# Kernel optimization log

Measured on AMD Instinct MI355X. Metric: run time of the kernel, lower is better.

The kernel has to match this reference:

```python
import jax, jax.numpy as jnp
import numpy as np

DIM = 384
NUM_HEADS = 6
HEAD_DIM = DIM // NUM_HEADS
SCALE = HEAD_DIM ** -0.5


def setup_inputs() -> dict:
    key = jax.random.key(0)
    k_x, k_qkvw, k_qkvb, k_pw, k_pb = jax.random.split(key, 5)
    B, N, C = 8, 2048, DIM
    x = jax.random.normal(k_x, (B, N, C), dtype=jnp.float32)
    # nn.Linear weights stored as (out, in); apply as x @ W.T + b
    s = 1.0 / np.sqrt(C)
    qkv_w = jax.random.uniform(k_qkvw, (3 * C, C), minval=-s, maxval=s, dtype=jnp.float32)
    qkv_b = jax.random.uniform(k_qkvb, (3 * C,), minval=-s, maxval=s, dtype=jnp.float32)
    proj_w = jax.random.uniform(k_pw, (C, C), minval=-s, maxval=s, dtype=jnp.float32)
    proj_b = jax.random.uniform(k_pb, (C,), minval=-s, maxval=s, dtype=jnp.float32)
    return {"x": x, "qkv_w": qkv_w, "qkv_b": qkv_b, "proj_w": proj_w,
            "proj_b": proj_b, "h": 64, "w": 32}


def reference(x, qkv_w, qkv_b, proj_w, proj_b, h, w):
    B, N, C = x.shape
    H, D = NUM_HEADS, HEAD_DIM
    qkv = x @ qkv_w.T + qkv_b              # [B, N, 3C]
    qkv = qkv.reshape(B, N, 3, H, D)
    q = qkv[:, :, 0].transpose(0, 2, 1, 3) * SCALE  # [B, H, N, D]
    k = qkv[:, :, 1].transpose(0, 2, 1, 3)
    v = qkv[:, :, 2].transpose(0, 2, 1, 3)
    attn = jnp.einsum('bhnd,bhmd->bhnm', q, k)      # [B, H, N, N]
    attn = jax.nn.softmax(attn, axis=-1)
    out = jnp.einsum('bhnm,bhmd->bhnd', attn, v)    # [B, H, N, D]
    out = out.transpose(0, 2, 1, 3).reshape(B, N, C)
    return out @ proj_w.T + proj_b
```

## Files before the change

### kernel.cpp

```cpp
#include <hip/hip_runtime.h>

typedef __attribute__((ext_vector_type(8))) short bf16x8;
typedef __attribute__((ext_vector_type(4))) float f32x4;
typedef __attribute__((ext_vector_type(16))) float f32x16;
typedef __attribute__((ext_vector_type(4))) unsigned int u32x4;

#define DIMC 384
#define NHEADS 6
#define HDIM 64
#define BATCH 8
#define SEQ 2048
#define TOKENS (BATCH*SEQ)
#define QKV_OUT (3*DIMC)

__device__ __forceinline__ unsigned short f2bf(float f) {
  unsigned int u = __float_as_uint(f);
  u += 0x7fffu + ((u >> 16) & 1u);
  return (unsigned short)(u >> 16);
}

__device__ __forceinline__ unsigned int cvt_pk_bf16(float a, float b) {
  unsigned int r;
  asm volatile("v_cvt_pk_bf16_f32 %0, %1, %2" : "=v"(r) : "v"(a), "v"(b));
  return r;
}

__device__ __forceinline__ void async_load16(const void* g, void* l) {
  __builtin_amdgcn_global_load_lds(
      (const __attribute__((address_space(1))) unsigned int*)g,
      (__attribute__((address_space(3))) unsigned int*)l, 16, 0, 0);
}

#define N4_X   (TOKENS*DIMC/4)
#define N4_W1  (QKV_OUT*DIMC/4)
#define N4_W2  (DIMC*DIMC/4)
__global__ void cast3_kernel(const float* __restrict__ x,
                             const float* __restrict__ w1,
                             const float* __restrict__ w2,
                             unsigned short* __restrict__ ox,
                             unsigned short* __restrict__ o1,
                             unsigned short* __restrict__ o2) {
  int i = blockIdx.x * blockDim.x + threadIdx.x;
  const int stride = gridDim.x * blockDim.x;
  for (; i < N4_X + N4_W1 + N4_W2; i += stride) {
    const float* src; unsigned short* dst; int j = i;
    if (j < N4_X)            { src = x;  dst = ox; }
    else if (j < N4_X+N4_W1) { j -= N4_X; src = w1; dst = o1; }
    else                     { j -= N4_X+N4_W1; src = w2; dst = o2; }
    float4 v = ((const float4*)src)[j];
    ushort4 o;
    o.x = f2bf(v.x); o.y = f2bf(v.y); o.z = f2bf(v.z); o.w = f2bf(v.w);
    ((ushort4*)dst)[j] = o;
  }
}

__global__ __launch_bounds__(256) void qkv_gemm_kernel(
    const unsigned short* __restrict__ A,
    const unsigned short* __restrict__ W,
    const float* __restrict__ bias,
    unsigned short* __restrict__ Qb,
    unsigned short* __restrict__ Kb,
    unsigned short* __restrict__ Vtb) {
  __shared__ unsigned short As[2][128*32];
  __shared__ unsigned short Bs[2][128*32];
  const int tid = threadIdx.x;
  const int w = tid >> 6, l = tid & 63;
  const int wm = w >> 1, wn = w & 1;
  const int q4 = l >> 4, r15 = l & 15;
  const int m0 = blockIdx.y * 128;
  const int n0 = blockIdx.x * 128;

  f32x4 acc[4][4];
#pragma unroll
  for (int i = 0; i < 4; i++)
#pragma unroll
    for (int j = 0; j < 4; j++) acc[i][j] = f32x4{0.f, 0.f, 0.f, 0.f};

  const int arow = l >> 2;
  const int achk = l & 3;
  const unsigned short* Asrc = A + (size_t)(m0 + w*16 + arow) * 384 + achk * 8;
  const unsigned short* Wsrc = W + (size_t)(n0 + w*16 + arow) * 384 + achk * 8;

#pragma unroll
  for (int cc = 0; cc < 2; ++cc) {
    async_load16(Asrc + cc*64*384, (char*)As[0] + cc*4096 + w*1024);
    async_load16(Wsrc + cc*64*384, (char*)Bs[0] + cc*4096 + w*1024);
  }

  for (int kt = 0; kt < 12; ++kt) {
    const int buf = kt & 1;
    if (kt < 11) {
#pragma unroll
      for (int cc = 0; cc < 2; ++cc) {
        async_load16(Asrc + (kt+1)*32 + cc*64*384, (char*)As[buf^1] + cc*4096 + w*1024);
        async_load16(Wsrc + (kt+1)*32 + cc*64*384, (char*)Bs[buf^1] + cc*4096 + w*1024);
      }
      asm volatile("s_waitcnt vmcnt(4)" ::: "memory");
    } else {
      asm volatile("s_waitcnt vmcnt(0)" ::: "memory");
    }
    __builtin_amdgcn_s_barrier();
    asm volatile("" ::: "memory");
    bf16x8 a[4], b[4];
#pragma unroll
    for (int mi = 0; mi < 4; mi++)
      a[mi] = *(const bf16x8*)(&As[buf][(wm*64 + mi*16 + r15)*32 + q4*8]);
#pragma unroll
    for (int ni = 0; ni < 4; ni++)
      b[ni] = *(const bf16x8*)(&Bs[buf][(wn*64 + ni*16 + r15)*32 + q4*8]);
    __builtin_amdgcn_s_setprio(1);
#pragma unroll
    for (int mi = 0; mi < 4; mi++)
#pragma unroll
      for (int ni = 0; ni < 4; ni++)
        acc[mi][ni] = __builtin_amdgcn_mfma_f32_16x16x32_bf16(
            a[mi], b[ni], acc[mi][ni], 0, 0, 0);
    __builtin_amdgcn_s_setprio(0);
    asm volatile("s_waitcnt lgkmcnt(0)" ::: "memory");
    __builtin_amdgcn_s_barrier();
    asm volatile("" ::: "memory");
  }
  const int c3 = blockIdx.x / 3;
  const int nrel0 = (blockIdx.x % 3) * 128 + wn * 64;
  if (c3 == 2) {
#pragma unroll
    for (int ni = 0; ni < 4; ni++) {
      int ncol = nrel0 + ni*16 + r15;
      float bv = bias[n0 + wn*64 + ni*16 + r15];
      int h = ncol >> 6, d = ncol & 63;
#pragma unroll
      for (int mi = 0; mi < 4; mi++) {
        int m = m0 + wm*64 + mi*16 + 4*q4;
        int bb = m >> 11, t = m & 2047;
        ushort4 pk;
        pk.x = f2bf(acc[mi][ni][0] + bv);
        pk.y = f2bf(acc[mi][ni][1] + bv);
        pk.z = f2bf(acc[mi][ni][2] + bv);
        pk.w = f2bf(acc[mi][ni][3] + bv);
        *(ushort4*)(Vtb + ((size_t)(bb*NHEADS + h)*HDIM + d)*SEQ + t) = pk;
      }
    }
  } else {
    unsigned short* D = (c3 == 0) ? Qb : Kb;
    const float scale = (c3 == 0) ? 0.125f * 1.4426950408889634f : 1.0f;
#pragma unroll
    for (int ni = 0; ni < 4; ni++) {
      int ncol = nrel0 + ni*16 + r15;
      float bv = bias[n0 + wn*64 + ni*16 + r15];
      int h = ncol >> 6, d = ncol & 63;
#pragma unroll
      for (int mi = 0; mi < 4; mi++) {
#pragma unroll
        for (int reg = 0; reg < 4; reg++) {
          int m = m0 + wm*64 + mi*16 + 4*q4 + reg;
          int bb = m >> 11, t = m & 2047;
          float v = (acc[mi][ni][reg] + bv) * scale;
          D[((size_t)(bb*NHEADS + h)*SEQ + t)*HDIM + d] = f2bf(v);
        }
      }
    }
  }
}

__global__ __launch_bounds__(256, 3) void flash_kernel(
    const unsigned short* __restrict__ Q, const unsigned short* __restrict__ K,
    const unsigned short* __restrict__ Vt, unsigned short* __restrict__ O2) {
  __shared__ unsigned short Ks[2][64*64];
  __shared__ unsigned short Vs[2][64*64];
  const int tid = threadIdx.x;
  const int w = tid >> 6, l = tid & 63;
  const int hl = l >> 5, l31 = l & 31, l7 = l & 7;
  const int wg = blockIdx.x;
  const int logical = (wg & 7) * 96 + (wg >> 3);
  const int qt = logical & 15, bh = logical >> 4;
  const unsigned short* Qp = Q  + (size_t)bh * SEQ * HDIM;
  const unsigned short* Kp = K  + (size_t)bh * SEQ * HDIM;
  const unsigned short* Vp = Vt + (size_t)bh * HDIM * SEQ;

  const int qrow = qt*128 + w*32 + l31;
  bf16x8 qf[4];
#pragma unroll
  for (int ks = 0; ks < 4; ks++)
    qf[ks] = *(const bf16x8*)(Qp + (size_t)qrow*HDIM + ks*16 + hl*8);

  const int srow = w*8 + (l >> 3);
  const int sch  = l7 ^ (l >> 3) ^ w;
  const unsigned short* Ksrc = Kp + (size_t)srow*HDIM + sch*8;
  const unsigned short* Vsrc = Vp + (size_t)srow*SEQ  + sch*8;
  char* kdst = (char*)&Ks[0][0] + w*1024;
  char* vdst = (char*)&Vs[0][0] + w*1024;

  const int swl = (l31 >> 3) & 3;
  int rdoff[4];
#pragma unroll
  for (int ks = 0; ks < 4; ks++)
    rdoff[ks] = l31*128 + (((ks*2 + hl) ^ l7 ^ swl) << 4);

  f32x16 o0 = {}, o1 = {};
  float l_run = 0.f;

  async_load16(Ksrc,           kdst);
  async_load16(Ksrc + 32*HDIM, kdst + 4096);
  async_load16(Vsrc,           vdst);
  async_load16(Vsrc + 32*SEQ,  vdst + 4096);

#pragma unroll 2
  for (int kt = 0; kt < 32; ++kt) {
    const int buf = kt & 1;
    const unsigned short* ksb = &Ks[buf][0];
    const unsigned short* vsb = &Vs[buf][0];
    if (kt < 31) {
      const unsigned short* ks_ = Ksrc + (size_t)(kt+1)*64*HDIM;
      const unsigned short* vs_ = Vsrc + (size_t)(kt+1)*64;
      char* kd = kdst + (buf^1)*8192;
      char* vd = vdst + (buf^1)*8192;
      async_load16(ks_,           kd);
      async_load16(ks_ + 32*HDIM, kd + 4096);
      async_load16(vs_,           vd);
      async_load16(vs_ + 32*SEQ,  vd + 4096);
      asm volatile("s_waitcnt vmcnt(4)" ::: "memory");
    } else {
      asm volatile("s_waitcnt vmcnt(0)" ::: "memory");
    }
    __builtin_amdgcn_s_barrier();
    asm volatile("" ::: "memory");

    f32x16 s0 = {}, s1 = {};
    __builtin_amdgcn_s_setprio(1);
#pragma unroll
    for (int ks = 0; ks < 4; ks++) {
      bf16x8 kf0 = *(const bf16x8*)((const char*)ksb + rdoff[ks]);
      bf16x8 kf1 = *(const bf16x8*)((const char*)ksb + 4096 + rdoff[ks]);
      s0 = __builtin_amdgcn_mfma_f32_32x32x16_bf16(kf0, qf[ks], s0, 0, 0, 0);
      s1 = __builtin_amdgcn_mfma_f32_32x32x16_bf16(kf1, qf[ks], s1, 0, 0, 0);
    }
    __builtin_amdgcn_s_setprio(0);

    unsigned int Y[2][4][2];
    float lsum = 0.f;
#pragma unroll
    for (int h = 0; h < 4; h++) {
      float a0 = __builtin_amdgcn_exp2f(s0[4*h+0]);
      float a1 = __builtin_amdgcn_exp2f(s0[4*h+1]);
      float a2 = __builtin_amdgcn_exp2f(s0[4*h+2]);
      float a3 = __builtin_amdgcn_exp2f(s0[4*h+3]);
      lsum += (a0+a1)+(a2+a3);
      Y[0][h][0] = cvt_pk_bf16(a0, a1);
      Y[0][h][1] = cvt_pk_bf16(a2, a3);
      float b0 = __builtin_amdgcn_exp2f(s1[4*h+0]);
      float b1 = __builtin_amdgcn_exp2f(s1[4*h+1]);
      float b2 = __builtin_amdgcn_exp2f(s1[4*h+2]);
      float b3 = __builtin_amdgcn_exp2f(s1[4*h+3]);
      lsum += (b0+b1)+(b2+b3);
      Y[1][h][0] = cvt_pk_bf16(b0, b1);
      Y[1][h][1] = cvt_pk_bf16(b2, b3);
    }
    l_run += lsum;

    bf16x8 pa[4];
#pragma unroll
    for (int ksl = 0; ksl < 4; ksl++) {
      const int kb = ksl >> 1, P2 = ksl & 1;
      unsigned int x0 = Y[kb][2*P2+0][0], x1 = Y[kb][2*P2+0][1];
      unsigned int y0 = Y[kb][2*P2+1][0], y1 = Y[kb][2*P2+1][1];
      asm volatile("v_permlane32_swap_b32 %0, %1" : "+v"(x0), "+v"(y0));
      asm volatile("v_permlane32_swap_b32 %0, %1" : "+v"(x1), "+v"(y1));
      u32x4 t; t[0] = x0; t[1] = x1; t[2] = y0; t[3] = y1;
      union { u32x4 u; bf16x8 b; } cvt; cvt.u = t;
      pa[ksl] = cvt.b;
    }

    __builtin_amdgcn_s_setprio(1);
#pragma unroll
    for (int ksl = 0; ksl < 4; ksl++) {
      bf16x8 vf0 = *(const bf16x8*)((const char*)vsb + rdoff[ksl]);
      bf16x8 vf1 = *(const bf16x8*)((const char*)vsb + 4096 + rdoff[ksl]);
      o0 = __builtin_amdgcn_mfma_f32_32x32x16_bf16(pa[ksl], vf0, o0, 0, 0, 0);
      o1 = __builtin_amdgcn_mfma_f32_32x32x16_bf16(pa[ksl], vf1, o1, 0, 0, 0);
    }
    __builtin_amdgcn_s_setprio(0);
    asm volatile("s_waitcnt lgkmcnt(0)" ::: "memory");
    __builtin_amdgcn_s_barrier();
    asm volatile("" ::: "memory");
  }

  l_run += __shfl_xor(l_run, 32, 64);
  const float linv = 1.0f / l_run;
  const int b = bh / NHEADS, h = bh % NHEADS;
#pragma unroll
  for (int reg = 0; reg < 16; reg++) {
    const int qr = (reg & 3) + 8*(reg >> 2) + 4*hl;
    const float lr = __shfl(linv, qr, 64);
    const int t = qt*128 + w*32 + qr;
    unsigned short* dst = O2 + ((size_t)(b*SEQ + t))*DIMC + h*HDIM;
    dst[l31]      = f2bf(o0[reg] * lr);
    dst[32 + l31] = f2bf(o1[reg] * lr);
  }
}

__global__ __launch_bounds__(256) void proj_gemm_kernel(
    const unsigned short* __restrict__ A,
    const unsigned short* __restrict__ W,
    const float* __restrict__ bias,
    float* __restrict__ out) {
  __shared__ unsigned short As[2][128*32];
  __shared__ unsigned short Bs[2][64*32];
  const int tid = threadIdx.x;
  const int w = tid >> 6, l = tid & 63;
  const int q4 = l >> 4, r15 = l & 15;
  const int m0 = blockIdx.y * 128;
  const int n0 = blockIdx.x * 64;

  f32x4 acc[2][4];
#pragma unroll
  for (int i = 0; i < 2; i++)
#pragma unroll
    for (int j = 0; j < 4; j++) acc[i][j] = f32x4{0.f, 0.f, 0.f, 0.f};

  const int arow = l >> 2;
  const int achk = l & 3;
  const unsigned short* Asrc = A + (size_t)(m0 + w*16 + arow) * 384 + achk * 8;
  const unsigned short* Wsrc = W + (size_t)(n0 + w*16 + arow) * 384 + achk * 8;

#pragma unroll
  for (int cc = 0; cc < 2; ++cc)
    async_load16(Asrc + cc*64*384, (char*)As[0] + cc*4096 + w*1024);
  async_load16(Wsrc, (char*)Bs[0] + w*1024);

  for (int kt = 0; kt < 12; ++kt) {
    const int buf = kt & 1;
    if (kt < 11) {
#pragma unroll
      for (int cc = 0; cc < 2; ++cc)
        async_load16(Asrc + (kt+1)*32 + cc*64*384, (char*)As[buf^1] + cc*4096 + w*1024);
      async_load16(Wsrc + (kt+1)*32, (char*)Bs[buf^1] + w*1024);
      asm volatile("s_waitcnt vmcnt(3)" ::: "memory");
    } else {
      asm volatile("s_waitcnt vmcnt(0)" ::: "memory");
    }
    __builtin_amdgcn_s_barrier();
    asm volatile("" ::: "memory");
    bf16x8 a[2], b[4];
#pragma unroll
    for (int mi = 0; mi < 2; mi++)
      a[mi] = *(const bf16x8*)(&As[buf][(w*32 + mi*16 + r15)*32 + q4*8]);
#pragma unroll
    for (int ni = 0; ni < 4; ni++)
      b[ni] = *(const bf16x8*)(&Bs[buf][(ni*16 + r15)*32 + q4*8]);
    __builtin_amdgcn_s_setprio(1);
#pragma unroll
    for (int mi = 0; mi < 2; mi++)
#pragma unroll
      for (int ni = 0; ni < 4; ni++)
        acc[mi][ni] = __builtin_amdgcn_mfma_f32_16x16x32_bf16(
            a[mi], b[ni], acc[mi][ni], 0, 0, 0);
    __builtin_amdgcn_s_setprio(0);
    asm volatile("s_waitcnt lgkmcnt(0)" ::: "memory");
    __builtin_amdgcn_s_barrier();
    asm volatile("" ::: "memory");
  }
#pragma unroll
  for (int ni = 0; ni < 4; ni++) {
    int ncol = n0 + ni*16 + r15;
    float bv = bias[ncol];
#pragma unroll
    for (int mi = 0; mi < 2; mi++) {
#pragma unroll
      for (int reg = 0; reg < 4; reg++) {
        int m = m0 + w*32 + mi*16 + 4*q4 + reg;
        out[(size_t)m * DIMC + ncol] = acc[mi][ni][reg] + bv;
      }
    }
  }
}

extern "C" void kernel_launch(void* const* d_in, const int* in_sizes, int n_in,
                              void* d_out, int out_size, void* d_ws, size_t ws_size,
                              hipStream_t stream) {
  const float* x      = (const float*)d_in[0];
  const float* qkv_w  = (const float*)d_in[1];
  const float* qkv_b  = (const float*)d_in[2];
  const float* proj_w = (const float*)d_in[3];
  const float* proj_b = (const float*)d_in[4];
  float* out = (float*)d_out;

  unsigned short* xbf   = (unsigned short*)d_ws;
  unsigned short* wqkv  = xbf   + (size_t)TOKENS * DIMC;
  unsigned short* wproj = wqkv  + (size_t)QKV_OUT * DIMC;
  unsigned short* Qb    = wproj + (size_t)DIMC * DIMC;
  unsigned short* Kb    = Qb    + (size_t)TOKENS * DIMC;
  unsigned short* Vtb   = Kb    + (size_t)TOKENS * DIMC;
  unsigned short* A2    = Vtb   + (size_t)TOKENS * DIMC;

  cast3_kernel<<<2048, 256, 0, stream>>>(x, qkv_w, proj_w, xbf, wqkv, wproj);
  qkv_gemm_kernel<<<dim3(9, 128), 256, 0, stream>>>(xbf, wqkv, qkv_b, Qb, Kb, Vtb);
  flash_kernel<<<768, 256, 0, stream>>>(Qb, Kb, Vtb, A2);
  proj_gemm_kernel<<<dim3(6, 128), 256, 0, stream>>>(A2, wproj, proj_b, out);
}
```

Measured before the change: 124.8 us.

## Split flash attention KV tiles across wave pairs with 64-row query tiles

Each flash workgroup now covers 64 query rows instead of 128. Four waves form two query halves by two key halves, and each wave processes 32 keys of every 64-key tile. Partial outputs and row sums from the second key half are merged through shared memory at the end, and the grid doubles to 1536 blocks with occupancy hint raised to 4. This aims for more parallelism and occupancy. In exchange, K/V staging per query row doubles, an extra reduction and syncthreads are added, and the softmax still has no max subtraction.

```diff
diff --git a/kernel.cpp b/kernel.cpp
--- a/kernel.cpp
+++ b/kernel.cpp
@@ -162,7 +162,7 @@
   }
 }
 
-__global__ __launch_bounds__(256, 3) void flash_kernel(
+__global__ __launch_bounds__(256, 4) void flash_kernel(
     const unsigned short* __restrict__ Q, const unsigned short* __restrict__ K,
     const unsigned short* __restrict__ Vt, unsigned short* __restrict__ O2) {
   __shared__ unsigned short Ks[2][64*64];
@@ -170,14 +170,15 @@
   const int tid = threadIdx.x;
   const int w = tid >> 6, l = tid & 63;
   const int hl = l >> 5, l31 = l & 31, l7 = l & 7;
+  const int qh = w >> 1, kh = w & 1;
   const int wg = blockIdx.x;
-  const int logical = (wg & 7) * 96 + (wg >> 3);
-  const int qt = logical & 15, bh = logical >> 4;
+  const int logical = (wg & 7) * 192 + (wg >> 3);
+  const int qt = logical & 31, bh = logical >> 5;
   const unsigned short* Qp = Q  + (size_t)bh * SEQ * HDIM;
   const unsigned short* Kp = K  + (size_t)bh * SEQ * HDIM;
   const unsigned short* Vp = Vt + (size_t)bh * HDIM * SEQ;
 
-  const int qrow = qt*128 + w*32 + l31;
+  const int qrow = qt*64 + qh*32 + l31;
   bf16x8 qf[4];
 #pragma unroll
   for (int ks = 0; ks < 4; ks++)
@@ -191,10 +192,16 @@
   char* vdst = (char*)&Vs[0][0] + w*1024;
 
   const int swl = (l31 >> 3) & 3;
-  int rdoff[4];
+  int rdk[4];
 #pragma unroll
   for (int ks = 0; ks < 4; ks++)
-    rdoff[ks] = l31*128 + (((ks*2 + hl) ^ l7 ^ swl) << 4);
+    rdk[ks] = (32*kh + l31)*128 + (((ks*2 + hl) ^ l7 ^ swl) << 4);
+  int rdv[4];
+#pragma unroll
+  for (int dh = 0; dh < 2; dh++)
+#pragma unroll
+    for (int P2 = 0; P2 < 2; P2++)
+      rdv[dh*2+P2] = (dh*32 + l31)*128 + (((4*kh + 2*P2 + hl) ^ l7 ^ swl) << 4);
 
   f32x16 o0 = {}, o1 = {};
   float l_run = 0.f;
@@ -207,8 +214,8 @@
 #pragma unroll 2
   for (int kt = 0; kt < 32; ++kt) {
     const int buf = kt & 1;
-    const unsigned short* ksb = &Ks[buf][0];
-    const unsigned short* vsb = &Vs[buf][0];
+    const char* ksb = (const char*)&Ks[buf][0];
+    const char* vsb = (const char*)&Vs[buf][0];
     if (kt < 31) {
       const unsigned short* ks_ = Ksrc + (size_t)(kt+1)*64*HDIM;
       const unsigned short* vs_ = Vsrc + (size_t)(kt+1)*64;
@@ -225,58 +232,48 @@
     __builtin_amdgcn_s_barrier();
     asm volatile("" ::: "memory");
 
-    f32x16 s0 = {}, s1 = {};
+    f32x16 s = {};
     __builtin_amdgcn_s_setprio(1);
 #pragma unroll
     for (int ks = 0; ks < 4; ks++) {
-      bf16x8 kf0 = *(const bf16x8*)((const char*)ksb + rdoff[ks]);
-      bf16x8 kf1 = *(const bf16x8*)((const char*)ksb + 4096 + rdoff[ks]);
-      s0 = __builtin_amdgcn_mfma_f32_32x32x16_bf16(kf0, qf[ks], s0, 0, 0, 0);
-      s1 = __builtin_amdgcn_mfma_f32_32x32x16_bf16(kf1, qf[ks], s1, 0, 0, 0);
+      bf16x8 kf = *(const bf16x8*)(ksb + rdk[ks]);
+      s = __builtin_amdgcn_mfma_f32_32x32x16_bf16(kf, qf[ks], s, 0, 0, 0);
     }
     __builtin_amdgcn_s_setprio(0);
 
-    unsigned int Y[2][4][2];
+    unsigned int Y[4][2];
     float lsum = 0.f;
 #pragma unroll
     for (int h = 0; h < 4; h++) {
-      float a0 = __builtin_amdgcn_exp2f(s0[4*h+0]);
-      float a1 = __builtin_amdgcn_exp2f(s0[4*h+1]);
-      float a2 = __builtin_amdgcn_exp2f(s0[4*h+2]);
-      float a3 = __builtin_amdgcn_exp2f(s0[4*h+3]);
+      float a0 = __builtin_amdgcn_exp2f(s[4*h+0]);
+      float a1 = __builtin_amdgcn_exp2f(s[4*h+1]);
+      float a2 = __builtin_amdgcn_exp2f(s[4*h+2]);
+      float a3 = __builtin_amdgcn_exp2f(s[4*h+3]);
       lsum += (a0+a1)+(a2+a3);
-      Y[0][h][0] = cvt_pk_bf16(a0, a1);
-      Y[0][h][1] = cvt_pk_bf16(a2, a3);
-      float b0 = __builtin_amdgcn_exp2f(s1[4*h+0]);
-      float b1 = __builtin_amdgcn_exp2f(s1[4*h+1]);
-      float b2 = __builtin_amdgcn_exp2f(s1[4*h+2]);
-      float b3 = __builtin_amdgcn_exp2f(s1[4*h+3]);
-      lsum += (b0+b1)+(b2+b3);
-      Y[1][h][0] = cvt_pk_bf16(b0, b1);
-      Y[1][h][1] = cvt_pk_bf16(b2, b3);
+      Y[h][0] = cvt_pk_bf16(a0, a1);
+      Y[h][1] = cvt_pk_bf16(a2, a3);
     }
     l_run += lsum;
 
-    bf16x8 pa[4];
-#pragma unroll
-    for (int ksl = 0; ksl < 4; ksl++) {
-      const int kb = ksl >> 1, P2 = ksl & 1;
-      unsigned int x0 = Y[kb][2*P2+0][0], x1 = Y[kb][2*P2+0][1];
-      unsigned int y0 = Y[kb][2*P2+1][0], y1 = Y[kb][2*P2+1][1];
+    bf16x8 pa[2];
+#pragma unroll
+    for (int P2 = 0; P2 < 2; P2++) {
+      unsigned int x0 = Y[2*P2+0][0], x1 = Y[2*P2+0][1];
+      unsigned int y0 = Y[2*P2+1][0], y1 = Y[2*P2+1][1];
       asm volatile("v_permlane32_swap_b32 %0, %1" : "+v"(x0), "+v"(y0));
       asm volatile("v_permlane32_swap_b32 %0, %1" : "+v"(x1), "+v"(y1));
       u32x4 t; t[0] = x0; t[1] = x1; t[2] = y0; t[3] = y1;
       union { u32x4 u; bf16x8 b; } cvt; cvt.u = t;
-      pa[ksl] = cvt.b;
+      pa[P2] = cvt.b;
     }
 
     __builtin_amdgcn_s_setprio(1);
 #pragma unroll
-    for (int ksl = 0; ksl < 4; ksl++) {
-      bf16x8 vf0 = *(const bf16x8*)((const char*)vsb + rdoff[ksl]);
-      bf16x8 vf1 = *(const bf16x8*)((const char*)vsb + 4096 + rdoff[ksl]);
-      o0 = __builtin_amdgcn_mfma_f32_32x32x16_bf16(pa[ksl], vf0, o0, 0, 0, 0);
-      o1 = __builtin_amdgcn_mfma_f32_32x32x16_bf16(pa[ksl], vf1, o1, 0, 0, 0);
+    for (int P2 = 0; P2 < 2; P2++) {
+      bf16x8 vf0 = *(const bf16x8*)(vsb + rdv[P2]);
+      bf16x8 vf1 = *(const bf16x8*)(vsb + rdv[2 + P2]);
+      o0 = __builtin_amdgcn_mfma_f32_32x32x16_bf16(pa[P2], vf0, o0, 0, 0, 0);
+      o1 = __builtin_amdgcn_mfma_f32_32x32x16_bf16(pa[P2], vf1, o1, 0, 0, 0);
     }
     __builtin_amdgcn_s_setprio(0);
     asm volatile("s_waitcnt lgkmcnt(0)" ::: "memory");
@@ -285,16 +282,33 @@
   }
 
   l_run += __shfl_xor(l_run, 32, 64);
-  const float linv = 1.0f / l_run;
-  const int b = bh / NHEADS, h = bh % NHEADS;
-#pragma unroll
-  for (int reg = 0; reg < 16; reg++) {
-    const int qr = (reg & 3) + 8*(reg >> 2) + 4*hl;
-    const float lr = __shfl(linv, qr, 64);
-    const int t = qt*128 + w*32 + qr;
-    unsigned short* dst = O2 + ((size_t)(b*SEQ + t))*DIMC + h*HDIM;
-    dst[l31]      = f2bf(o0[reg] * lr);
-    dst[32 + l31] = f2bf(o1[reg] * lr);
+
+  float* sO = (float*)&Ks[0][0];
+  float* sL = (float*)&Vs[0][0];
+  if (kh == 1) {
+#pragma unroll
+    for (int reg = 0; reg < 16; reg++) {
+      const int qr = (reg & 3) + 8*(reg >> 2) + 4*hl;
+      sO[qh*2048 + qr*64 + l31]      = o0[reg];
+      sO[qh*2048 + qr*64 + 32 + l31] = o1[reg];
+    }
+    if (hl == 0) sL[qh*32 + l31] = l_run;
+  }
+  __syncthreads();
+  if (kh == 0) {
+    const float linv = 1.0f / (l_run + sL[qh*32 + l31]);
+    const int b = bh / NHEADS, h = bh % NHEADS;
+#pragma unroll
+    for (int reg = 0; reg < 16; reg++) {
+      const int qr = (reg & 3) + 8*(reg >> 2) + 4*hl;
+      const float lr = __shfl(linv, qr, 64);
+      const float v0 = o0[reg] + sO[qh*2048 + qr*64 + l31];
+      const float v1 = o1[reg] + sO[qh*2048 + qr*64 + 32 + l31];
+      const int t = qt*64 + qh*32 + qr;
+      unsigned short* dst = O2 + ((size_t)(b*SEQ + t))*DIMC + h*HDIM;
+      dst[l31]      = f2bf(v0 * lr);
+      dst[32 + l31] = f2bf(v1 * lr);
+    }
   }
 }
 
@@ -394,6 +408,6 @@
 
   cast3_kernel<<<2048, 256, 0, stream>>>(x, qkv_w, proj_w, xbf, wqkv, wproj);
   qkv_gemm_kernel<<<dim3(9, 128), 256, 0, stream>>>(xbf, wqkv, qkv_b, Qb, Kb, Vtb);
-  flash_kernel<<<768, 256, 0, stream>>>(Qb, Kb, Vtb, A2);
+  flash_kernel<<<1536, 256, 0, stream>>>(Qb, Kb, Vtb, A2);
   proj_gemm_kernel<<<dim3(6, 128), 256, 0, stream>>>(A2, wproj, proj_b, out);
 }
```

Measured after the change: 132.3 us. +6.0%, slower.

## Load K/V fragments directly from global memory, dropping LDS staging and padding V^T rows

Applied to the files above, without the earlier changes.

The flash kernel no longer stages K and V tiles through double-buffered shared memory with async global-to-LDS loads. Each wave now reads its MFMA operand fragments straight from global memory into registers, relying on L2/L1 reuse across waves and workgroups. The V^T buffer gets a padded row stride (2080) to avoid cache set conflicts on the strided row reads. This removes the LDS traffic and most of the synchronisation, but each of the four waves now fetches the same K/V data separately and loses explicit prefetch overlap. A leftover per-iteration barrier remains.

```diff
diff --git a/kernel.cpp b/kernel.cpp
--- a/kernel.cpp
+++ b/kernel.cpp
@@ -12,6 +12,7 @@
 #define SEQ 2048
 #define TOKENS (BATCH*SEQ)
 #define QKV_OUT (3*DIMC)
+#define VTP 2080
 
 __device__ __forceinline__ unsigned short f2bf(float f) {
   unsigned int u = __float_as_uint(f);
@@ -137,7 +138,7 @@
         pk.y = f2bf(acc[mi][ni][1] + bv);
         pk.z = f2bf(acc[mi][ni][2] + bv);
         pk.w = f2bf(acc[mi][ni][3] + bv);
-        *(ushort4*)(Vtb + ((size_t)(bb*NHEADS + h)*HDIM + d)*SEQ + t) = pk;
+        *(ushort4*)(Vtb + ((size_t)(bb*NHEADS + h)*HDIM + d)*VTP + t) = pk;
       }
     }
   } else {
@@ -165,17 +166,15 @@
 __global__ __launch_bounds__(256, 3) void flash_kernel(
     const unsigned short* __restrict__ Q, const unsigned short* __restrict__ K,
     const unsigned short* __restrict__ Vt, unsigned short* __restrict__ O2) {
-  __shared__ unsigned short Ks[2][64*64];
-  __shared__ unsigned short Vs[2][64*64];
   const int tid = threadIdx.x;
   const int w = tid >> 6, l = tid & 63;
-  const int hl = l >> 5, l31 = l & 31, l7 = l & 7;
+  const int hl = l >> 5, l31 = l & 31;
   const int wg = blockIdx.x;
   const int logical = (wg & 7) * 96 + (wg >> 3);
   const int qt = logical & 15, bh = logical >> 4;
   const unsigned short* Qp = Q  + (size_t)bh * SEQ * HDIM;
   const unsigned short* Kp = K  + (size_t)bh * SEQ * HDIM;
-  const unsigned short* Vp = Vt + (size_t)bh * HDIM * SEQ;
+  const unsigned short* Vp = Vt + (size_t)bh * HDIM * VTP;
 
   const int qrow = qt*128 + w*32 + l31;
   bf16x8 qf[4];
@@ -183,58 +182,40 @@
   for (int ks = 0; ks < 4; ks++)
     qf[ks] = *(const bf16x8*)(Qp + (size_t)qrow*HDIM + ks*16 + hl*8);
 
-  const int srow = w*8 + (l >> 3);
-  const int sch  = l7 ^ (l >> 3) ^ w;
-  const unsigned short* Ksrc = Kp + (size_t)srow*HDIM + sch*8;
-  const unsigned short* Vsrc = Vp + (size_t)srow*SEQ  + sch*8;
-  char* kdst = (char*)&Ks[0][0] + w*1024;
-  char* vdst = (char*)&Vs[0][0] + w*1024;
-
-  const int swl = (l31 >> 3) & 3;
-  int rdoff[4];
-#pragma unroll
-  for (int ks = 0; ks < 4; ks++)
-    rdoff[ks] = l31*128 + (((ks*2 + hl) ^ l7 ^ swl) << 4);
+  const unsigned short* krow0 = Kp + (size_t)l31*HDIM      + hl*8;
+  const unsigned short* krow1 = Kp + (size_t)(32+l31)*HDIM + hl*8;
+  const unsigned short* vrow0 = Vp + (size_t)l31*VTP      + hl*8;
+  const unsigned short* vrow1 = Vp + (size_t)(32+l31)*VTP + hl*8;
 
   f32x16 o0 = {}, o1 = {};
   float l_run = 0.f;
 
-  async_load16(Ksrc,           kdst);
-  async_load16(Ksrc + 32*HDIM, kdst + 4096);
-  async_load16(Vsrc,           vdst);
-  async_load16(Vsrc + 32*SEQ,  vdst + 4096);
-
-#pragma unroll 2
   for (int kt = 0; kt < 32; ++kt) {
-    const int buf = kt & 1;
-    const unsigned short* ksb = &Ks[buf][0];
-    const unsigned short* vsb = &Vs[buf][0];
-    if (kt < 31) {
-      const unsigned short* ks_ = Ksrc + (size_t)(kt+1)*64*HDIM;
-      const unsigned short* vs_ = Vsrc + (size_t)(kt+1)*64;
-      char* kd = kdst + (buf^1)*8192;
-      char* vd = vdst + (buf^1)*8192;
-      async_load16(ks_,           kd);
-      async_load16(ks_ + 32*HDIM, kd + 4096);
-      async_load16(vs_,           vd);
-      async_load16(vs_ + 32*SEQ,  vd + 4096);
-      asm volatile("s_waitcnt vmcnt(4)" ::: "memory");
-    } else {
-      asm volatile("s_waitcnt vmcnt(0)" ::: "memory");
-    }
-    __builtin_amdgcn_s_barrier();
-    asm volatile("" ::: "memory");
+    const size_t koff = (size_t)kt*64*HDIM;
+    const size_t voff = (size_t)kt*64;
+
+    bf16x8 kf0[4], kf1[4];
+#pragma unroll
+    for (int ks = 0; ks < 4; ks++) {
+      kf0[ks] = *(const bf16x8*)(krow0 + koff + ks*16);
+      kf1[ks] = *(const bf16x8*)(krow1 + koff + ks*16);
+    }
 
     f32x16 s0 = {}, s1 = {};
     __builtin_amdgcn_s_setprio(1);
 #pragma unroll
     for (int ks = 0; ks < 4; ks++) {
-      bf16x8 kf0 = *(const bf16x8*)((const char*)ksb + rdoff[ks]);
-      bf16x8 kf1 = *(const bf16x8*)((const char*)ksb + 4096 + rdoff[ks]);
-      s0 = __builtin_amdgcn_mfma_f32_32x32x16_bf16(kf0, qf[ks], s0, 0, 0, 0);
-      s1 = __builtin_amdgcn_mfma_f32_32x32x16_bf16(kf1, qf[ks], s1, 0, 0, 0);
+      s0 = __builtin_amdgcn_mfma_f32_32x32x16_bf16(kf0[ks], qf[ks], s0, 0, 0, 0);
+      s1 = __builtin_amdgcn_mfma_f32_32x32x16_bf16(kf1[ks], qf[ks], s1, 0, 0, 0);
     }
     __builtin_amdgcn_s_setprio(0);
+
+    bf16x8 vf0[4], vf1[4];
+#pragma unroll
+    for (int ks = 0; ks < 4; ks++) {
+      vf0[ks] = *(const bf16x8*)(vrow0 + voff + ks*16);
+      vf1[ks] = *(const bf16x8*)(vrow1 + voff + ks*16);
+    }
 
     unsigned int Y[2][4][2];
     float lsum = 0.f;
@@ -273,15 +254,12 @@
     __builtin_amdgcn_s_setprio(1);
 #pragma unroll
     for (int ksl = 0; ksl < 4; ksl++) {
-      bf16x8 vf0 = *(const bf16x8*)((const char*)vsb + rdoff[ksl]);
-      bf16x8 vf1 = *(const bf16x8*)((const char*)vsb + 4096 + rdoff[ksl]);
-      o0 = __builtin_amdgcn_mfma_f32_32x32x16_bf16(pa[ksl], vf0, o0, 0, 0, 0);
-      o1 = __builtin_amdgcn_mfma_f32_32x32x16_bf16(pa[ksl], vf1, o1, 0, 0, 0);
+      o0 = __builtin_amdgcn_mfma_f32_32x32x16_bf16(pa[ksl], vf0[ksl], o0, 0, 0, 0);
+      o1 = __builtin_amdgcn_mfma_f32_32x32x16_bf16(pa[ksl], vf1[ksl], o1, 0, 0, 0);
     }
     __builtin_amdgcn_s_setprio(0);
-    asm volatile("s_waitcnt lgkmcnt(0)" ::: "memory");
-    __builtin_amdgcn_s_barrier();
-    asm volatile("" ::: "memory");
+
+    __builtin_amdgcn_s_barrier();
   }
 
   l_run += __shfl_xor(l_run, 32, 64);
@@ -390,7 +368,7 @@
   unsigned short* Qb    = wproj + (size_t)DIMC * DIMC;
   unsigned short* Kb    = Qb    + (size_t)TOKENS * DIMC;
   unsigned short* Vtb   = Kb    + (size_t)TOKENS * DIMC;
-  unsigned short* A2    = Vtb   + (size_t)TOKENS * DIMC;
+  unsigned short* A2    = Vtb   + (size_t)48 * HDIM * VTP;
 
   cast3_kernel<<<2048, 256, 0, stream>>>(x, qkv_w, proj_w, xbf, wqkv, wproj);
   qkv_gemm_kernel<<<dim3(9, 128), 256, 0, stream>>>(xbf, wqkv, qkv_b, Qb, Kb, Vtb);
```

Result: slower. 199.0 us (+59.5%).

## Triple-buffer LDS tiles to drop trailing barrier in QKV GEMM and flash loops

Applied to the files above, without the earlier changes.

Both the QKV GEMM and the flash-attention kernel move from double to triple LDS buffers with a rotating index. This lets each iteration drop its end-of-loop lgkmcnt wait and second barrier, leaving one barrier per iteration. A third buffer means a prefetch never overwrites the tile other waves may still be reading. The cost is 50% more LDS per block, which could lower occupancy in the flash kernel (launch bounds ask for 3 blocks/CU), and the loop no longer has explicit unroll 2.

```diff
diff --git a/kernel.cpp b/kernel.cpp
--- a/kernel.cpp
+++ b/kernel.cpp
@@ -61,8 +61,8 @@
     unsigned short* __restrict__ Qb,
     unsigned short* __restrict__ Kb,
     unsigned short* __restrict__ Vtb) {
-  __shared__ unsigned short As[2][128*32];
-  __shared__ unsigned short Bs[2][128*32];
+  __shared__ unsigned short As[3][128*32];
+  __shared__ unsigned short Bs[3][128*32];
   const int tid = threadIdx.x;
   const int w = tid >> 6, l = tid & 63;
   const int wm = w >> 1, wn = w & 1;
@@ -83,17 +83,18 @@
 
 #pragma unroll
   for (int cc = 0; cc < 2; ++cc) {
-    async_load16(Asrc + cc*64*384, (char*)As[0] + cc*4096 + w*1024);
-    async_load16(Wsrc + cc*64*384, (char*)Bs[0] + cc*4096 + w*1024);
-  }
-
+    async_load16(Asrc + cc*64*384, (char*)&As[0][0] + cc*4096 + w*1024);
+    async_load16(Wsrc + cc*64*384, (char*)&Bs[0][0] + cc*4096 + w*1024);
+  }
+
+  int cur = 0;
   for (int kt = 0; kt < 12; ++kt) {
-    const int buf = kt & 1;
+    const int nxt = (cur == 2) ? 0 : cur + 1;
     if (kt < 11) {
 #pragma unroll
       for (int cc = 0; cc < 2; ++cc) {
-        async_load16(Asrc + (kt+1)*32 + cc*64*384, (char*)As[buf^1] + cc*4096 + w*1024);
-        async_load16(Wsrc + (kt+1)*32 + cc*64*384, (char*)Bs[buf^1] + cc*4096 + w*1024);
+        async_load16(Asrc + (kt+1)*32 + cc*64*384, (char*)&As[0][0] + nxt*8192 + cc*4096 + w*1024);
+        async_load16(Wsrc + (kt+1)*32 + cc*64*384, (char*)&Bs[0][0] + nxt*8192 + cc*4096 + w*1024);
       }
       asm volatile("s_waitcnt vmcnt(4)" ::: "memory");
     } else {
@@ -101,13 +102,15 @@
     }
     __builtin_amdgcn_s_barrier();
     asm volatile("" ::: "memory");
+    const unsigned short* asb = &As[0][0] + cur*4096;
+    const unsigned short* bsb = &Bs[0][0] + cur*4096;
     bf16x8 a[4], b[4];
 #pragma unroll
     for (int mi = 0; mi < 4; mi++)
-      a[mi] = *(const bf16x8*)(&As[buf][(wm*64 + mi*16 + r15)*32 + q4*8]);
+      a[mi] = *(const bf16x8*)(asb + (wm*64 + mi*16 + r15)*32 + q4*8);
 #pragma unroll
     for (int ni = 0; ni < 4; ni++)
-      b[ni] = *(const bf16x8*)(&Bs[buf][(wn*64 + ni*16 + r15)*32 + q4*8]);
+      b[ni] = *(const bf16x8*)(bsb + (wn*64 + ni*16 + r15)*32 + q4*8);
     __builtin_amdgcn_s_setprio(1);
 #pragma unroll
     for (int mi = 0; mi < 4; mi++)
@@ -116,9 +119,7 @@
         acc[mi][ni] = __builtin_amdgcn_mfma_f32_16x16x32_bf16(
             a[mi], b[ni], acc[mi][ni], 0, 0, 0);
     __builtin_amdgcn_s_setprio(0);
-    asm volatile("s_waitcnt lgkmcnt(0)" ::: "memory");
-    __builtin_amdgcn_s_barrier();
-    asm volatile("" ::: "memory");
+    cur = nxt;
   }
   const int c3 = blockIdx.x / 3;
   const int nrel0 = (blockIdx.x % 3) * 128 + wn * 64;
@@ -165,8 +166,8 @@
 __global__ __launch_bounds__(256, 3) void flash_kernel(
     const unsigned short* __restrict__ Q, const unsigned short* __restrict__ K,
     const unsigned short* __restrict__ Vt, unsigned short* __restrict__ O2) {
-  __shared__ unsigned short Ks[2][64*64];
-  __shared__ unsigned short Vs[2][64*64];
+  __shared__ unsigned short Ks[3][64*64];
+  __shared__ unsigned short Vs[3][64*64];
   const int tid = threadIdx.x;
   const int w = tid >> 6, l = tid & 63;
   const int hl = l >> 5, l31 = l & 31, l7 = l & 7;
@@ -187,8 +188,6 @@
   const int sch  = l7 ^ (l >> 3) ^ w;
   const unsigned short* Ksrc = Kp + (size_t)srow*HDIM + sch*8;
   const unsigned short* Vsrc = Vp + (size_t)srow*SEQ  + sch*8;
-  char* kdst = (char*)&Ks[0][0] + w*1024;
-  char* vdst = (char*)&Vs[0][0] + w*1024;
 
   const int swl = (l31 >> 3) & 3;
   int rdoff[4];
@@ -199,21 +198,19 @@
   f32x16 o0 = {}, o1 = {};
   float l_run = 0.f;
 
-  async_load16(Ksrc,           kdst);
-  async_load16(Ksrc + 32*HDIM, kdst + 4096);
-  async_load16(Vsrc,           vdst);
-  async_load16(Vsrc + 32*SEQ,  vdst + 4096);
-
-#pragma unroll 2
+  async_load16(Ksrc,           (char*)&Ks[0][0] + w*1024);
+  async_load16(Ksrc + 32*HDIM, (char*)&Ks[0][0] + w*1024 + 4096);
+  async_load16(Vsrc,           (char*)&Vs[0][0] + w*1024);
+  async_load16(Vsrc + 32*SEQ,  (char*)&Vs[0][0] + w*1024 + 4096);
+
+  int cur = 0;
   for (int kt = 0; kt < 32; ++kt) {
-    const int buf = kt & 1;
-    const unsigned short* ksb = &Ks[buf][0];
-    const unsigned short* vsb = &Vs[buf][0];
+    const int nxt = (cur == 2) ? 0 : cur + 1;
     if (kt < 31) {
       const unsigned short* ks_ = Ksrc + (size_t)(kt+1)*64*HDIM;
       const unsigned short* vs_ = Vsrc + (size_t)(kt+1)*64;
-      char* kd = kdst + (buf^1)*8192;
-      char* vd = vdst + (buf^1)*8192;
+      char* kd = (char*)&Ks[0][0] + nxt*8192 + w*1024;
+      char* vd = (char*)&Vs[0][0] + nxt*8192 + w*1024;
       async_load16(ks_,           kd);
       async_load16(ks_ + 32*HDIM, kd + 4096);
       async_load16(vs_,           vd);
@@ -225,12 +222,15 @@
     __builtin_amdgcn_s_barrier();
     asm volatile("" ::: "memory");
 
+    const char* ksb = (const char*)&Ks[0][0] + cur*8192;
+    const char* vsb = (const char*)&Vs[0][0] + cur*8192;
+
     f32x16 s0 = {}, s1 = {};
     __builtin_amdgcn_s_setprio(1);
 #pragma unroll
     for (int ks = 0; ks < 4; ks++) {
-      bf16x8 kf0 = *(const bf16x8*)((const char*)ksb + rdoff[ks]);
-      bf16x8 kf1 = *(const bf16x8*)((const char*)ksb + 4096 + rdoff[ks]);
+      bf16x8 kf0 = *(const bf16x8*)(ksb + rdoff[ks]);
+      bf16x8 kf1 = *(const bf16x8*)(ksb + 4096 + rdoff[ks]);
       s0 = __builtin_amdgcn_mfma_f32_32x32x16_bf16(kf0, qf[ks], s0, 0, 0, 0);
       s1 = __builtin_amdgcn_mfma_f32_32x32x16_bf16(kf1, qf[ks], s1, 0, 0, 0);
     }
@@ -273,15 +273,13 @@
     __builtin_amdgcn_s_setprio(1);
 #pragma unroll
     for (int ksl = 0; ksl < 4; ksl++) {
-      bf16x8 vf0 = *(const bf16x8*)((const char*)vsb + rdoff[ksl]);
-      bf16x8 vf1 = *(const bf16x8*)((const char*)vsb + 4096 + rdoff[ksl]);
+      bf16x8 vf0 = *(const bf16x8*)(vsb + rdoff[ksl]);
+      bf16x8 vf1 = *(const bf16x8*)(vsb + 4096 + rdoff[ksl]);
       o0 = __builtin_amdgcn_mfma_f32_32x32x16_bf16(pa[ksl], vf0, o0, 0, 0, 0);
       o1 = __builtin_amdgcn_mfma_f32_32x32x16_bf16(pa[ksl], vf1, o1, 0, 0, 0);
     }
     __builtin_amdgcn_s_setprio(0);
-    asm volatile("s_waitcnt lgkmcnt(0)" ::: "memory");
-    __builtin_amdgcn_s_barrier();
-    asm volatile("" ::: "memory");
+    cur = nxt;
   }
 
   l_run += __shfl_xor(l_run, 32, 64);
```

Measured after the change: 124.1 us. No clear change (-0.6%).
